# Optimization experiments

Hardware: AMD Instinct MI355X
Metric: run time of the kernel (lower is better)

The kernel has to match this reference:

```python
import jax, jax.numpy as jnp
import numpy as np

NC = 2            # num_classes
CONF_THR = 0.7
IOU_THR = 0.2

_PI, _PJ = np.triu_indices(9, k=1)   # 36 candidate edge directions for min-area rect


def _decode_level(out, stride):
    # out: [C,h,w]; scale (x,y) channels by stride and add the pixel grid, flatten to [h*w, C]
    C, h, w = out.shape
    gw = (stride * jnp.arange(w, dtype=out.dtype))[None, :]
    gh = (stride * jnp.arange(h, dtype=out.dtype))[:, None]
    out = out.at[NC + 1].set(out[NC + 1] * stride + gw)
    out = out.at[NC + 2].set(out[NC + 2] * stride + gh)
    return out.reshape(C, -1).T


def _min_area_polygons(pts18):
    # pts18: (N,18) interleaved (a,b) coordinate pairs of 9 points.
    # Min-area enclosing rectangle: optimal rect is aligned with some point-pair direction;
    # brute-force all 36 pairs (superset of hull edges) -> exact result, fully vectorized.
    P = pts18.reshape(-1, 9, 2)                       # (N,9,2)
    d = P[:, _PJ] - P[:, _PI]                         # (N,36,2)
    nrm = jnp.sqrt(jnp.sum(d * d, -1) + 1e-12)
    c, s = d[..., 0] / nrm, d[..., 1] / nrm           # (N,36)
    a, b = P[..., 0][:, None, :], P[..., 1][:, None, :]   # (N,1,9)
    u = a * c[..., None] + b * s[..., None]           # rotate by -theta
    v = -a * s[..., None] + b * c[..., None]
    umin, umax = u.min(-1), u.max(-1)
    vmin, vmax = v.min(-1), v.max(-1)
    area = (umax - umin) * (vmax - vmin)              # (N,36)
    k = jnp.argmin(area, 1)[:, None]
    tk = lambda z: jnp.take_along_axis(z, k, 1)[:, 0]
    c, s, umin, umax, vmin, vmax = map(tk, (c, s, umin, umax, vmin, vmax))
    cu = jnp.stack([umin, umax, umax, umin], -1)      # rect corners in rotated frame
    cv = jnp.stack([vmin, vmin, vmax, vmax], -1)
    ca = cu * c[:, None] - cv * s[:, None]            # rotate back
    cb = cu * s[:, None] + cv * c[:, None]
    return jnp.stack([ca, cb], -1).reshape(-1, 8)     # (N,8) interleaved corners


def _points_in_quad(pts, quad):
    # pts (M,2), quad (4,2) convex with consistent winding -> (M,) bool
    e = jnp.roll(quad, -1, 0) - quad
    r = pts[:, None, :] - quad[None]
    cr = e[None, :, 0] * r[..., 1] - e[None, :, 1] * r[..., 0]
    return (cr >= 0).all(-1) | (cr <= 0).all(-1)


def _box_decoder(rect):
    # rect (N,8) -> (N,5) [cx, cy, w, h, angle]; y_first=True convention from the source
    w = jnp.sqrt((rect[:, 0] - rect[:, 2]) ** 2 + (rect[:, 1] - rect[:, 3]) ** 2)
    h = jnp.sqrt((rect[:, 4] - rect[:, 2]) ** 2 + (rect[:, 5] - rect[:, 3]) ** 2)
    cx = rect[:, 1:8:2].sum(1) * 0.25
    cy = rect[:, 0:8:2].sum(1) * 0.25
    ang = jnp.arctan((rect[:, 0] - rect[:, 2]) / (rect[:, 1] - rect[:, 3]))
    return jnp.stack([cx, cy, w, h, ang], -1)


def _rbox_corners(b):
    cx, cy, w, h, a = b[0], b[1], b[2], b[3], b[4]
    cs, sn = jnp.cos(a), jnp.sin(a)
    lx = jnp.array([-0.5, 0.5, 0.5, -0.5]) * w
    ly = jnp.array([-0.5, -0.5, 0.5, 0.5]) * h
    return jnp.stack([cx + lx * cs - ly * sn, cy + lx * sn + ly * cs], -1)  # (4,2)


def _quad_inter_area(A, B):
    # exact intersection area of two convex quads A,B (4,2):
    # candidates = corners of each inside the other + all 16 edge-edge intersections,
    # sorted by angle around their centroid, masked shoelace.
    inA = _points_in_quad(B, A)
    inB = _points_in_quad(A, B)
    rA = jnp.roll(A, -1, 0) - A
    rB = jnp.roll(B, -1, 0) - B
    qp = B[None] - A[:, None]                                  # (4,4,2)
    den = rA[:, None, 0] * rB[None, :, 1] - rA[:, None, 1] * rB[None, :, 0]
    dsafe = jnp.where(jnp.abs(den) < 1e-9, 1e-9, den)
    t = (qp[..., 0] * rB[None, :, 1] - qp[..., 1] * rB[None, :, 0]) / dsafe
    uu = (qp[..., 0] * rA[:, None, 1] - qp[..., 1] * rA[:, None, 0]) / dsafe
    okx = (jnp.abs(den) > 1e-9) & (t >= 0) & (t <= 1) & (uu >= 0) & (uu <= 1)
    X = A[:, None] + t[..., None] * rA[:, None]
    pts = jnp.concatenate([A, B, X.reshape(16, 2)], 0)          # (24,2)
    val = jnp.concatenate([inB, inA, okx.reshape(16)], 0)
    n = val.sum()
    cen = jnp.sum(jnp.where(val[:, None], pts, 0.0), 0) / jnp.maximum(n, 1)
    rel = pts - cen
    ang = jnp.where(val, jnp.arctan2(rel[:, 1], rel[:, 0]), 1e9)
    o = jnp.argsort(ang)
    rp, vs = rel[o], val[o]
    rp = jnp.where(vs[:, None], rp, rp[0])   # invalid slots -> first valid vertex (zero-area edges)
    nx = jnp.roll(rp, -1, 0)
    area = 0.5 * jnp.abs(jnp.sum(rp[:, 0] * nx[:, 1] - rp[:, 1] * nx[:, 0]))
    return jnp.where(n >= 3, area, 0.0)


def _forward(out3, out4, out5, off1_l3, off1_l4, off1_l5, offf_l3, offf_l4, offf_l5):
    outs = jnp.concatenate([_decode_level(out3[0], 4),
                            _decode_level(out4[0], 8),
                            _decode_level(out5[0], 16)], 0)          # (N, NC+3)
    flat = lambda z: z[0].reshape(18, -1).T
    off1 = jnp.concatenate([flat(off1_l3), flat(off1_l4), flat(off1_l5)], 0)
    offf = jnp.concatenate([flat(offf_l3), flat(offf_l4), flat(offf_l5)], 0) + off1
    N = outs.shape[0]
    x, y = outs[:, NC + 1], outs[:, NC + 2]
    offf = offf + jnp.tile(jnp.stack([y, x], -1), (1, 9))            # (y,x) interleaved, 9 points
    xs, ys = offf[:, 1:18:2], offf[:, 0:18:2]
    area = (xs.max(1) - xs.min(1)) * (ys.max(1) - ys.min(1)) / 40.0
    conf = outs[:, 0]
    conf_mask = conf > CONF_THR * jax.nn.sigmoid(area)
    rect = _min_area_polygons(offf)                                  # (N,8)
    boxes5 = _box_decoder(rect)                                      # (N,5)
    corners = jax.vmap(_rbox_corners)(boxes5)                        # (N,4,2)
    areas5 = boxes5[:, 2] * boxes5[:, 3]
    position = outs[:, NC + 1:]                                      # (N,2) = (x,y)
    pts_yx = jnp.stack([position[:, 1], position[:, 0]], -1)         # (y,x), matches rect plane
    quads = rect.reshape(N, 4, 2)
    order = jnp.argsort(jnp.where(conf_mask, conf, -jnp.inf))[::-1]

    def step(carry, i):
        suppressed, keep = carry
        active = jnp.logical_not(suppressed[i])
        keep = keep.at[i].set(active)
        inside = _points_in_quad(pts_yx, quads[i])                   # points_in_polygons
        inter = jax.vmap(lambda C: _quad_inter_area(corners[i], C))(corners)
        iou = inter / (areas5[i] + areas5 - inter + 1e-9)            # box_iou_rotated
        suppressed = suppressed | (active & (inside | (iou >= IOU_THR)))
        return (suppressed, keep), None

    init = (jnp.logical_not(conf_mask), jnp.zeros(N, dtype=bool))
    (_, keep), _ = jax.lax.scan(step, init, order)

    cls = outs[:, 1:NC + 1]
    maxc = cls.max(1)
    masks = jnp.stack([keep & (cls[:, i] == maxc) for i in range(NC)], 0)  # (NC,N)
    cnt = masks.sum(1)
    result = jnp.where(masks[:, :, None], position[None], 0.0)             # (NC,N,2) padded
    rect_out = rect * keep[:, None].astype(rect.dtype)                     # (N,8) padded
    return cnt, result, rect_out


def setup_inputs() -> dict:
    key = jax.random.key(0)
    shapes = [("out3", (1, NC + 3, 32, 32)), ("out4", (1, NC + 3, 16, 16)), ("out5", (1, NC + 3, 8, 8)),
              ("off1_l3", (1, 18, 32, 32)), ("off1_l4", (1, 18, 16, 16)), ("off1_l5", (1, 18, 8, 8)),
              ("offf_l3", (1, 18, 32, 32)), ("offf_l4", (1, 18, 16, 16)), ("offf_l5", (1, 18, 8, 8))]
    ks = jax.random.split(key, len(shapes))
    return {n: jax.random.normal(k, s, dtype=jnp.float32) for (n, s), k in zip(shapes, ks)}


def reference(out3, out4, out5, off1_l3, off1_l4, off1_l5, offf_l3, offf_l4, offf_l5):
    return _forward(out3, out4, out5, off1_l3, off1_l4, off1_l5, offf_l3, offf_l4, offf_l5)
```

## Files before the change

### kernel.cpp

```cpp
#include <hip/hip_runtime.h>
#include <math.h>

#define N_DET 1344
#define NW 21
#define MW_MAX 8
#define T2S 9
#define PAIR_CAP 40000


__device__ __forceinline__ bool pt_in_quad4(const float* qx, const float* qy,
                                            float px, float py) {
    bool allp = true, alln = true;
#pragma unroll
    for (int k = 0; k < 4; k++) {
        int k1 = (k + 1) & 3;
        float ex = qx[k1] - qx[k], ey = qy[k1] - qy[k];
        float rx = px - qx[k],     ry = py - qy[k];
        float cr = ex * ry - ey * rx;
        allp = allp && (cr >= 0.f);
        alln = alln && (cr <= 0.f);
    }
    return allp || alln;
}

__device__ float quad_inter_area(const float* Ax, const float* Ay,
                                 const float* Bx, const float* By) {
    float px[24], py[24];
    unsigned vmask = 0;
    int n = 0;
#pragma unroll
    for (int k = 0; k < 4; k++) {
        px[k] = Ax[k]; py[k] = Ay[k];
        if (pt_in_quad4(Bx, By, Ax[k], Ay[k])) { vmask |= 1u << k; n++; }
    }
#pragma unroll
    for (int k = 0; k < 4; k++) {
        px[4 + k] = Bx[k]; py[4 + k] = By[k];
        if (pt_in_quad4(Ax, Ay, Bx[k], By[k])) { vmask |= 1u << (4 + k); n++; }
    }
#pragma unroll
    for (int k = 0; k < 4; k++) {
        int k1 = (k + 1) & 3;
        float rax = Ax[k1] - Ax[k], ray = Ay[k1] - Ay[k];
#pragma unroll
        for (int l = 0; l < 4; l++) {
            int l1 = (l + 1) & 3;
            float rbx = Bx[l1] - Bx[l], rby = By[l1] - By[l];
            float qpx = Bx[l] - Ax[k],  qpy = By[l] - Ay[k];
            float den = rax * rby - ray * rbx;
            float ad  = fabsf(den);
            float dsafe = (ad < 1e-9f) ? 1e-9f : den;
            float t = (qpx * rby - qpy * rbx) / dsafe;
            float u = (qpx * ray - qpy * rax) / dsafe;
            bool ok = (ad > 1e-9f) && t >= 0.f && t <= 1.f && u >= 0.f && u <= 1.f;
            int id = 8 + k * 4 + l;
            px[id] = Ax[k] + t * rax;
            py[id] = Ay[k] + t * ray;
            if (ok) { vmask |= 1u << id; n++; }
        }
    }
    float cx = 0.f, cy = 0.f;
#pragma unroll
    for (int m = 0; m < 24; m++)
        if ((vmask >> m) & 1u) { cx += px[m]; cy += py[m]; }
    int mx = (n < 1) ? 1 : n;
    cx = cx / (float)mx;
    cy = cy / (float)mx;

    unsigned long long key[32];
    float sx[32], sy[32];
#pragma unroll
    for (int m = 0; m < 24; m++) {
        float rx = px[m] - cx, ry = py[m] - cy;
        float a = ((vmask >> m) & 1u) ? atan2f(ry, rx) : 1e9f;
        unsigned u = __float_as_uint(a);
        u = (u & 0x80000000u) ? ~u : (u | 0x80000000u);
        key[m] = (((unsigned long long)u) << 6) | (unsigned)m;
        sx[m] = rx; sy[m] = ry;
    }
#pragma unroll
    for (int m = 24; m < 32; m++) { key[m] = ~0ull; sx[m] = 0.f; sy[m] = 0.f; }

#pragma unroll
    for (int k = 2; k <= 32; k <<= 1) {
#pragma unroll
        for (int j = k >> 1; j > 0; j >>= 1) {
#pragma unroll
            for (int t = 0; t < 32; t++) {
                int l = t ^ j;
                if (l > t) {
                    bool up = ((t & k) == 0);
                    bool sw = up ? (key[t] > key[l]) : (key[t] < key[l]);
                    if (sw) {
                        unsigned long long tk = key[t]; key[t] = key[l]; key[l] = tk;
                        float tx = sx[t]; sx[t] = sx[l]; sx[l] = tx;
                        float ty = sy[t]; sy[t] = sy[l]; sy[l] = ty;
                    }
                }
            }
        }
    }

    unsigned ut = __float_as_uint(1e9f) | 0x80000000u;
    unsigned long long kt = ((unsigned long long)ut) << 6;
    float fx = sx[0], fy = sy[0];
    float qx2[24], qy2[24];
#pragma unroll
    for (int m = 0; m < 24; m++) {
        bool v = key[m] < kt;
        qx2[m] = v ? sx[m] : fx;
        qy2[m] = v ? sy[m] : fy;
    }
    float ssum = 0.f;
#pragma unroll
    for (int m = 0; m < 24; m++) {
        int m1 = (m + 1) % 24;
        ssum += qx2[m] * qy2[m1] - qy2[m] * qx2[m1];
    }
    float area = 0.5f * fabsf(ssum);
    return (n >= 3) ? area : 0.f;
}

__device__ bool iou_suppress(const float* __restrict__ cor, const float* __restrict__ a5,
                             int i, int j) {
    float Axr[4], Ayr[4], Bxr[4], Byr[4];
#pragma unroll
    for (int k = 0; k < 4; k++) {
        Axr[k] = cor[i * 8 + 2 * k]; Ayr[k] = cor[i * 8 + 2 * k + 1];
        Bxr[k] = cor[j * 8 + 2 * k]; Byr[k] = cor[j * 8 + 2 * k + 1];
    }
    float inter = quad_inter_area(Axr, Ayr, Bxr, Byr);
    float iou = inter / (a5[i] + a5[j] - inter + 1e-9f);
    return iou >= 0.2f;
}

__global__ void k_decode(const float* __restrict__ out3, const float* __restrict__ out4,
                         const float* __restrict__ out5,
                         const float* __restrict__ o1l3, const float* __restrict__ o1l4,
                         const float* __restrict__ o1l5,
                         const float* __restrict__ ofl3, const float* __restrict__ ofl4,
                         const float* __restrict__ ofl5,
                         float* conf, float* cls0, float* cls1, float* xx, float* yy,
                         float* a5, float* ccx, float* ccy, float* rr,
                         float* rect, float* cor, int* mask, int* Mcnt, int* pairCnt) {
    int n = blockIdx.x * blockDim.x + threadIdx.x;
    if (n >= N_DET) return;
    if (n == 0) { *Mcnt = 0; *pairCnt = 0; }
    const float *out, *o1, *of;
    int w, idx; float stride;
    if (n < 1024)      { out = out3; o1 = o1l3; of = ofl3; w = 32; idx = n;        stride = 4.f; }
    else if (n < 1280) { out = out4; o1 = o1l4; of = ofl4; w = 16; idx = n - 1024; stride = 8.f; }
    else               { out = out5; o1 = o1l5; of = ofl5; w = 8;  idx = n - 1280; stride = 16.f; }
    int hw = w * w;
    int row = idx / w, col = idx % w;
    float cf = out[0 * hw + idx];
    float c0 = out[1 * hw + idx];
    float c1 = out[2 * hw + idx];
    float x  = out[3 * hw + idx] * stride + stride * (float)col;
    float y  = out[4 * hw + idx] * stride + stride * (float)row;

    float Pa[9], Pb[9];
    float minb = INFINITY, maxb = -INFINITY, mina = INFINITY, maxa = -INFINITY;
#pragma unroll
    for (int k = 0; k < 9; k++) {
        float a = of[(2 * k) * hw + idx]     + o1[(2 * k) * hw + idx]     + y;
        float b = of[(2 * k + 1) * hw + idx] + o1[(2 * k + 1) * hw + idx] + x;
        Pa[k] = a; Pb[k] = b;
        mina = fminf(mina, a); maxa = fmaxf(maxa, a);
        minb = fminf(minb, b); maxb = fmaxf(maxb, b);
    }
    float area = (maxb - minb) * (maxa - mina) / 40.0f;
    float sg = 1.0f / (1.0f + expf(-area));
    int m = (cf > 0.7f * sg) ? 1 : 0;

    float best = INFINITY, bc = 0.f, bs = 0.f;
    float bumin = 0.f, bumax = 0.f, bvmin = 0.f, bvmax = 0.f;
#pragma unroll
    for (int i = 0; i < 9; i++) {
#pragma unroll
        for (int j = i + 1; j < 9; j++) {
            float d0 = Pa[j] - Pa[i], d1 = Pb[j] - Pb[i];
            float nr = sqrtf(d0 * d0 + d1 * d1 + 1e-12f);
            float c = d0 / nr, s = d1 / nr;
            float umin = INFINITY, umax = -INFINITY, vmin = INFINITY, vmax = -INFINITY;
#pragma unroll
            for (int k = 0; k < 9; k++) {
                float u =  Pa[k] * c + Pb[k] * s;
                float v = -Pa[k] * s + Pb[k] * c;
                umin = fminf(umin, u); umax = fmaxf(umax, u);
                vmin = fminf(vmin, v); vmax = fmaxf(vmax, v);
            }
            float ar = (umax - umin) * (vmax - vmin);
            if (ar < best) { best = ar; bc = c; bs = s;
                             bumin = umin; bumax = umax; bvmin = vmin; bvmax = vmax; }
        }
    }
    float cu[4] = {bumin, bumax, bumax, bumin};
    float cv[4] = {bvmin, bvmin, bvmax, bvmax};
    float r8[8];
#pragma unroll
    for (int k = 0; k < 4; k++) {
        r8[2 * k]     = cu[k] * bc - cv[k] * bs;
        r8[2 * k + 1] = cu[k] * bs + cv[k] * bc;
    }
    float w5 = sqrtf((r8[0] - r8[2]) * (r8[0] - r8[2]) + (r8[1] - r8[3]) * (r8[1] - r8[3]));
    float h5 = sqrtf((r8[4] - r8[2]) * (r8[4] - r8[2]) + (r8[5] - r8[3]) * (r8[5] - r8[3]));
    float cx = (r8[1] + r8[3] + r8[5] + r8[7]) * 0.25f;
    float cy = (r8[0] + r8[2] + r8[4] + r8[6]) * 0.25f;
    float ang = atanf((r8[0] - r8[2]) / (r8[1] - r8[3]));
    float cs = cosf(ang), sn = sinf(ang);
    const float lxs[4] = {-0.5f, 0.5f, 0.5f, -0.5f};
    const float lys[4] = {-0.5f, -0.5f, 0.5f, 0.5f};
#pragma unroll
    for (int k = 0; k < 4; k++) {
        cor[n * 8 + 2 * k]     = cx + lxs[k] * w5 * cs - lys[k] * h5 * sn;
        cor[n * 8 + 2 * k + 1] = cy + lxs[k] * w5 * sn + lys[k] * h5 * cs;
    }
#pragma unroll
    for (int k = 0; k < 8; k++) rect[n * 8 + k] = r8[k];
    conf[n] = cf; cls0[n] = c0; cls1[n] = c1;
    xx[n] = x; yy[n] = y; a5[n] = w5 * h5; mask[n] = m;
    ccx[n] = cx; ccy[n] = cy;
    rr[n] = 0.5f * sqrtf(w5 * w5 + h5 * h5);
}

__global__ __launch_bounds__(64) void k_order(const float* __restrict__ conf,
                                              const int* __restrict__ mask,
                                              int* order, int* Mcnt) {
    int b = blockIdx.x;
    int lane = threadIdx.x;
    int mb = mask[b];
    float ki = mb ? conf[b] : -INFINITY;
    int rank = 0;
    for (int j = lane; j < N_DET; j += 64) {
        float kj = mask[j] ? conf[j] : -INFINITY;
        rank += ((kj > ki) || (kj == ki && j > b)) ? 1 : 0;
    }
    for (int off = 32; off; off >>= 1) rank += __shfl_down(rank, off, 64);
    if (lane == 0) {
        order[rank] = b;
        if (mb) atomicAdd(Mcnt, 1);
    }
}

__global__ __launch_bounds__(256) void k_pairs_a(
        const float* __restrict__ rect, const float* __restrict__ cor,
        const float* __restrict__ a5,
        const float* __restrict__ xx, const float* __restrict__ yy,
        const float* __restrict__ ccx, const float* __restrict__ ccy,
        const float* __restrict__ rr,
        const int* __restrict__ order, const int* __restrict__ Mcnt,
        unsigned long long* __restrict__ S2, unsigned int* __restrict__ pairs,
        int* __restrict__ pairCnt) {
    int M = *Mcnt;
    if (M <= 0) return;
    int MW = (M + 63) >> 6;
    bool use_list = (MW <= MW_MAX);
    int lane  = threadIdx.x & 63;
    int gwave = (blockIdx.x * 256 + threadIdx.x) >> 6;
    int nwave = (gridDim.x * 256) >> 6;
    int total = M * MW;
    for (int t = gwave; t < total; t += nwave) {
        int p = t / MW;
        int w = t - p * MW;
        int i = order[p];
        int q = w * 64 + lane;
        bool valid = q < M;
        int j = valid ? order[q] : i;

        float cbi = ccx[i], cai = ccy[i], ri = rr[i];
        float da = yy[j] - cai, db = xx[j] - cbi;
        float rin = ri + 0.1f;
        bool inside = false;
        if (da * da + db * db <= rin * rin) {
            float qxr[4], qyr[4];
#pragma unroll
            for (int k = 0; k < 4; k++) { qxr[k] = rect[i * 8 + 2 * k]; qyr[k] = rect[i * 8 + 2 * k + 1]; }
            inside = pt_in_quad4(qxr, qyr, yy[j], xx[j]);
        }
        bool bit = valid && inside;
        unsigned long long bb = __ballot(bit);
        if (lane == 0) S2[p * MW + w] = bb;

        float ex = cbi - ccx[j], ey = cai - ccy[j];
        float rs = ri + rr[j] + 0.1f;
        bool iou_pos = valid && (q != p) && !bit && (ex * ex + ey * ey <= rs * rs);
        if (use_list) {
            unsigned long long pm = __ballot(iou_pos);
            if (pm) {
                int cw = __popcll(pm);
                int base = 0;
                if (lane == 0) base = atomicAdd(pairCnt, cw);
                base = __shfl(base, 0, 64);
                if (iou_pos) {
                    int pos = base + __popcll(pm & ((1ull << lane) - 1ull));
                    if (pos < PAIR_CAP) {
                        pairs[pos] = ((unsigned)p << 11) | (unsigned)q;
                    } else if (iou_suppress(cor, a5, i, j)) {
                        atomicOr(&S2[p * MW + w], 1ull << (q & 63));
                    }
                }
            }
        } else if (iou_pos) {
            if (iou_suppress(cor, a5, i, j))
                atomicOr(&S2[p * MW + w], 1ull << (q & 63));
        }
    }
}

__global__ __launch_bounds__(256) void k_pairs_b(
        const float* __restrict__ cor, const float* __restrict__ a5,
        const int* __restrict__ order, const int* __restrict__ Mcnt,
        const int* __restrict__ pairCnt, const unsigned int* __restrict__ pairs,
        unsigned long long* __restrict__ S2) {
    int M = *Mcnt;
    int MW = (M + 63) >> 6;
    if (MW > MW_MAX) return;
    int cnt = *pairCnt; if (cnt > PAIR_CAP) cnt = PAIR_CAP;
    int stride = gridDim.x * 256;
    for (int t = blockIdx.x * 256 + threadIdx.x; t < cnt; t += stride) {
        unsigned v = pairs[t];
        int p = (int)(v >> 11), q = (int)(v & 2047u);
        int i = order[p], j = order[q];
        if (iou_suppress(cor, a5, i, j))
            atomicOr(&S2[p * MW + (q >> 6)], 1ull << (q & 63));
    }
}

__global__ __launch_bounds__(512) void k_scan_out(
    const float* __restrict__ cls0, const float* __restrict__ cls1,
    const float* __restrict__ xx, const float* __restrict__ yy,
    const float* __restrict__ rect,
    const int* __restrict__ order, const int* __restrict__ Mcnt,
    const unsigned long long* __restrict__ S2, float* __restrict__ out) {
    __shared__ int order_s[N_DET];
    __shared__ unsigned long long T2[512 * T2S];
    __shared__ unsigned long long Kfin[MW_MAX];
    __shared__ unsigned int keep32[(N_DET + 31) / 32];
    __shared__ int cnt_s[2];
    int tid = threadIdx.x;
    int lane = tid & 63, wid = tid >> 6;
    int M = *Mcnt;
    int MW = (M + 63) >> 6;
    for (int t = tid; t < N_DET; t += 512) order_s[t] = order[t];
    for (int t = tid; t < (N_DET + 31) / 32; t += 512) keep32[t] = 0u;
    if (tid < 2) cnt_s[tid] = 0;
    if (tid < MW_MAX) Kfin[tid] = 0ull;
    __syncthreads();

    if (M > 0 && MW <= MW_MAX) {
        for (int blk = wid; blk < MW * MW; blk += 8) {
            int wp = blk / MW, wq = blk - wp * MW;
            int pp = wp * 64 + lane;
            unsigned long long x = (pp < M) ? S2[pp * MW + wq] : 0ull;
#pragma unroll
            for (int b = 0; b < 64; b++) {
                unsigned long long bb = __ballot((x >> b) & 1ull);
                if (lane == b) T2[(wq * 64 + b) * T2S + wp] = bb;
            }
        }
        __syncthreads();

        if (wid == 0) {
            unsigned long long kw[MW_MAX];
#pragma unroll
            for (int w = 0; w < MW_MAX; w++) {
                int lo = w * 64;
                kw[w] = (M > lo) ? ((M - lo >= 64) ? ~0ull : ((1ull << (M - lo)) - 1ull)) : 0ull;
            }
            unsigned long long pmask = lane ? ((1ull << lane) - 1ull) : 0ull;
            for (int it = 0; it <= M; ++it) {
                bool changed = false;
#pragma unroll
                for (int k = 0; k < MW_MAX; k++) {
                    if (k < MW) {
                        int q = k * 64 + lane;
                        const unsigned long long* row = &T2[q * T2S];
                        unsigned long long sup = 0ull;
#pragma unroll
                        for (int w = 0; w < MW_MAX; w++) {
                            if (w < k)       sup |= row[w] & kw[w];
                            else if (w == k) sup |= row[w] & kw[w] & pmask;
                        }
                        bool nb = (q < M) && (sup == 0ull);
                        unsigned long long nw = __ballot(nb);
                        changed |= (nw != kw[k]);
                        kw[k] = nw;
                    }
                }
                if (!changed) break;
            }
            if (lane == 0) {
#pragma unroll
                for (int w = 0; w < MW_MAX; w++) Kfin[w] = kw[w];
            }
        }
        __syncthreads();
        for (int t = tid; t < M; t += 512) {
            if ((Kfin[t >> 6] >> (t & 63)) & 1ull) {
                int i = order_s[t];
                atomicOr(&keep32[i >> 5], 1u << (i & 31));
            }
        }
    } else if (M > 0) {
        if (wid == 0) {
            unsigned long long rem = 0ull;
            int lo = lane * 64;
            if (M > lo) rem = (M - lo >= 64) ? ~0ull : ((1ull << (M - lo)) - 1ull);
            for (int guard = 0; guard < N_DET; guard++) {
                unsigned long long vote = __ballot(rem != 0ull);
                if (!vote) break;
                int w = __builtin_ctzll(vote);
                unsigned long long wd = __shfl(rem, w, 64);
                int b = __builtin_ctzll(wd);
                int p = w * 64 + b;
                int i = order_s[p];
                if (lane == 0) atomicOr(&keep32[i >> 5], 1u << (i & 31));
                unsigned long long rowv = (lane < MW) ? S2[p * MW + lane] : 0ull;
                rem &= ~rowv;
                if (lane == w) rem &= ~(1ull << b);
            }
        }
    }
    __syncthreads();

    int c0 = 0, c1 = 0;
    for (int n = tid; n < N_DET; n += 512) {
        bool kp = (keep32[n >> 5] >> (n & 31)) & 1u;
        float a = cls0[n], b = cls1[n];
        float mxc = fmaxf(a, b);
        bool m0 = kp && (a == mxc);
        bool m1 = kp && (b == mxc);
        float x = xx[n], y = yy[n];
        out[2 + 0 * N_DET * 2 + n * 2 + 0] = m0 ? x : 0.f;
        out[2 + 0 * N_DET * 2 + n * 2 + 1] = m0 ? y : 0.f;
        out[2 + 1 * N_DET * 2 + n * 2 + 0] = m1 ? x : 0.f;
        out[2 + 1 * N_DET * 2 + n * 2 + 1] = m1 ? y : 0.f;
        float kf = kp ? 1.f : 0.f;
#pragma unroll
        for (int k = 0; k < 8; k++)
            out[2 + 2 * N_DET * 2 + n * 8 + k] = rect[n * 8 + k] * kf;
        c0 += m0 ? 1 : 0;
        c1 += m1 ? 1 : 0;
    }
    if (c0) atomicAdd(&cnt_s[0], c0);
    if (c1) atomicAdd(&cnt_s[1], c1);
    __syncthreads();
    if (tid == 0) { out[0] = (float)cnt_s[0]; out[1] = (float)cnt_s[1]; }
}

extern "C" void kernel_launch(void* const* d_in, const int* in_sizes, int n_in,
                              void* d_out, int out_size, void* d_ws, size_t ws_size,
                              hipStream_t stream) {
    const float* out3 = (const float*)d_in[0];
    const float* out4 = (const float*)d_in[1];
    const float* out5 = (const float*)d_in[2];
    const float* o1l3 = (const float*)d_in[3];
    const float* o1l4 = (const float*)d_in[4];
    const float* o1l5 = (const float*)d_in[5];
    const float* ofl3 = (const float*)d_in[6];
    const float* ofl4 = (const float*)d_in[7];
    const float* ofl5 = (const float*)d_in[8];
    float* out = (float*)d_out;

    const int N = N_DET;
    float* wsf  = (float*)d_ws;
    float* conf = wsf + 0 * N;
    float* cls0 = wsf + 1 * N;
    float* cls1 = wsf + 2 * N;
    float* xx   = wsf + 3 * N;
    float* yy   = wsf + 4 * N;
    float* a5   = wsf + 5 * N;
    float* ccx  = wsf + 6 * N;
    float* ccy  = wsf + 7 * N;
    float* rr   = wsf + 8 * N;
    float* rect = wsf + 9 * N;
    float* cor  = wsf + 17 * N;
    int* mask   = (int*)(wsf + 25 * N);
    int* order  = mask + N;
    int* Mcnt   = order + N;
    int* pairCnt = Mcnt + 1;
    unsigned long long* S2 = (unsigned long long*)(wsf + 27 * N + 4);
    unsigned int* pairs = (unsigned int*)((char*)S2 + 32768);

    k_decode<<<(N + 255) / 256, 256, 0, stream>>>(out3, out4, out5, o1l3, o1l4, o1l5,
                                                  ofl3, ofl4, ofl5,
                                                  conf, cls0, cls1, xx, yy, a5,
                                                  ccx, ccy, rr, rect, cor, mask, Mcnt, pairCnt);
    k_order<<<N, 64, 0, stream>>>(conf, mask, order, Mcnt);
    k_pairs_a<<<1024, 256, 0, stream>>>(rect, cor, a5, xx, yy, ccx, ccy, rr,
                                        order, Mcnt, S2, pairs, pairCnt);
    k_pairs_b<<<64, 256, 0, stream>>>(cor, a5, order, Mcnt, pairCnt, pairs, S2);
    k_scan_out<<<1, 512, 0, stream>>>(cls0, cls1, xx, yy, rect, order, Mcnt, S2, out);
}
```

Before: 142.9 us.

## Scatter per-box data into sorted order and fuse pair kernels via shared-memory queue

The sort kernel now also scatters box attributes (centers, radii, areas, rects, corners) into rank-ordered compacted arrays, so the pair kernel indexes them directly instead of going through order[] indirection. The two pair kernels are merged into one: candidate IoU pairs are queued in a per-block shared-memory queue and evaluated after a block barrier rather than through a global list processed by a second launch. The grid drops from 1024 to 256 blocks, and the mask is folded into a single key array. This removes one launch, the global pair buffer and its atomic counter, at the cost of extra scatter writes in the sort kernel and the risk that a block's queue overflows into inline evaluation.

```diff
diff --git a/kernel.cpp b/kernel.cpp
--- a/kernel.cpp
+++ b/kernel.cpp
@@ -2,10 +2,9 @@
 #include <math.h>
 
 #define N_DET 1344
-#define NW 21
 #define MW_MAX 8
 #define T2S 9
-#define PAIR_CAP 40000
+#define QCAP 2048
 
 
 __device__ __forceinline__ bool pt_in_quad4(const float* qx, const float* qy,
@@ -121,16 +120,16 @@
     return (n >= 3) ? area : 0.f;
 }
 
-__device__ bool iou_suppress(const float* __restrict__ cor, const float* __restrict__ a5,
-                             int i, int j) {
+__device__ bool iou_suppress_c(const float* __restrict__ co_cor,
+                               const float* __restrict__ co_a5, int p, int q) {
     float Axr[4], Ayr[4], Bxr[4], Byr[4];
 #pragma unroll
     for (int k = 0; k < 4; k++) {
-        Axr[k] = cor[i * 8 + 2 * k]; Ayr[k] = cor[i * 8 + 2 * k + 1];
-        Bxr[k] = cor[j * 8 + 2 * k]; Byr[k] = cor[j * 8 + 2 * k + 1];
+        Axr[k] = co_cor[p * 8 + 2 * k]; Ayr[k] = co_cor[p * 8 + 2 * k + 1];
+        Bxr[k] = co_cor[q * 8 + 2 * k]; Byr[k] = co_cor[q * 8 + 2 * k + 1];
     }
     float inter = quad_inter_area(Axr, Ayr, Bxr, Byr);
-    float iou = inter / (a5[i] + a5[j] - inter + 1e-9f);
+    float iou = inter / (co_a5[p] + co_a5[q] - inter + 1e-9f);
     return iou >= 0.2f;
 }
 
@@ -140,12 +139,12 @@
                          const float* __restrict__ o1l5,
                          const float* __restrict__ ofl3, const float* __restrict__ ofl4,
                          const float* __restrict__ ofl5,
-                         float* conf, float* cls0, float* cls1, float* xx, float* yy,
+                         float* keyArr, float* cls0, float* cls1, float* xx, float* yy,
                          float* a5, float* ccx, float* ccy, float* rr,
-                         float* rect, float* cor, int* mask, int* Mcnt, int* pairCnt) {
+                         float* rect, float* cor, int* Mcnt) {
     int n = blockIdx.x * blockDim.x + threadIdx.x;
     if (n >= N_DET) return;
-    if (n == 0) { *Mcnt = 0; *pairCnt = 0; }
+    if (n == 0) *Mcnt = 0;
     const float *out, *o1, *of;
     int w, idx; float stride;
     if (n < 1024)      { out = out3; o1 = o1l3; of = ofl3; w = 32; idx = n;        stride = 4.f; }
@@ -218,112 +217,128 @@
     }
 #pragma unroll
     for (int k = 0; k < 8; k++) rect[n * 8 + k] = r8[k];
-    conf[n] = cf; cls0[n] = c0; cls1[n] = c1;
-    xx[n] = x; yy[n] = y; a5[n] = w5 * h5; mask[n] = m;
+    keyArr[n] = m ? cf : -INFINITY;
+    cls0[n] = c0; cls1[n] = c1;
+    xx[n] = x; yy[n] = y; a5[n] = w5 * h5;
     ccx[n] = cx; ccy[n] = cy;
     rr[n] = 0.5f * sqrtf(w5 * w5 + h5 * h5);
 }
 
-__global__ __launch_bounds__(64) void k_order(const float* __restrict__ conf,
-                                              const int* __restrict__ mask,
-                                              int* order, int* Mcnt) {
+__global__ __launch_bounds__(64) void k_order(
+        const float* __restrict__ keyArr,
+        const float* __restrict__ xx, const float* __restrict__ yy,
+        const float* __restrict__ a5, const float* __restrict__ ccx,
+        const float* __restrict__ ccy, const float* __restrict__ rr,
+        const float* __restrict__ rect, const float* __restrict__ cor,
+        int* order, int* Mcnt,
+        float* co_ccx, float* co_ccy, float* co_rr, float* co_a5,
+        float* co_xx, float* co_yy, float* co_rect, float* co_cor) {
     int b = blockIdx.x;
     int lane = threadIdx.x;
-    int mb = mask[b];
-    float ki = mb ? conf[b] : -INFINITY;
+    float ki = keyArr[b];
     int rank = 0;
     for (int j = lane; j < N_DET; j += 64) {
-        float kj = mask[j] ? conf[j] : -INFINITY;
+        float kj = keyArr[j];
         rank += ((kj > ki) || (kj == ki && j > b)) ? 1 : 0;
     }
     for (int off = 32; off; off >>= 1) rank += __shfl_down(rank, off, 64);
+    rank = __shfl(rank, 0, 64);
     if (lane == 0) {
         order[rank] = b;
-        if (mb) atomicAdd(Mcnt, 1);
-    }
-}
-
-__global__ __launch_bounds__(256) void k_pairs_a(
-        const float* __restrict__ rect, const float* __restrict__ cor,
-        const float* __restrict__ a5,
-        const float* __restrict__ xx, const float* __restrict__ yy,
-        const float* __restrict__ ccx, const float* __restrict__ ccy,
-        const float* __restrict__ rr,
-        const int* __restrict__ order, const int* __restrict__ Mcnt,
-        unsigned long long* __restrict__ S2, unsigned int* __restrict__ pairs,
-        int* __restrict__ pairCnt) {
+        if (ki != -INFINITY) atomicAdd(Mcnt, 1);
+    }
+    if (lane < 8)            co_cor[rank * 8 + lane]        = cor[b * 8 + lane];
+    else if (lane < 16)      co_rect[rank * 8 + (lane - 8)] = rect[b * 8 + (lane - 8)];
+    else if (lane == 16)     co_ccx[rank] = ccx[b];
+    else if (lane == 17)     co_ccy[rank] = ccy[b];
+    else if (lane == 18)     co_rr[rank]  = rr[b];
+    else if (lane == 19)     co_a5[rank]  = a5[b];
+    else if (lane == 20)     co_xx[rank]  = xx[b];
+    else if (lane == 21)     co_yy[rank]  = yy[b];
+}
+
+__global__ __launch_bounds__(256) void k_pairs(
+        const float* __restrict__ co_rect, const float* __restrict__ co_cor,
+        const float* __restrict__ co_a5,
+        const float* __restrict__ co_xx, const float* __restrict__ co_yy,
+        const float* __restrict__ co_ccx, const float* __restrict__ co_ccy,
+        const float* __restrict__ co_rr,
+        const int* __restrict__ Mcnt, unsigned long long* __restrict__ S2) {
+    __shared__ unsigned int queue[QCAP];
+    __shared__ int qn;
     int M = *Mcnt;
-    if (M <= 0) return;
     int MW = (M + 63) >> 6;
-    bool use_list = (MW <= MW_MAX);
-    int lane  = threadIdx.x & 63;
-    int gwave = (blockIdx.x * 256 + threadIdx.x) >> 6;
-    int nwave = (gridDim.x * 256) >> 6;
-    int total = M * MW;
-    for (int t = gwave; t < total; t += nwave) {
-        int p = t / MW;
-        int w = t - p * MW;
-        int i = order[p];
-        int q = w * 64 + lane;
-        bool valid = q < M;
-        int j = valid ? order[q] : i;
-
-        float cbi = ccx[i], cai = ccy[i], ri = rr[i];
-        float da = yy[j] - cai, db = xx[j] - cbi;
-        float rin = ri + 0.1f;
-        bool inside = false;
-        if (da * da + db * db <= rin * rin) {
-            float qxr[4], qyr[4];
-#pragma unroll
-            for (int k = 0; k < 4; k++) { qxr[k] = rect[i * 8 + 2 * k]; qyr[k] = rect[i * 8 + 2 * k + 1]; }
-            inside = pt_in_quad4(qxr, qyr, yy[j], xx[j]);
-        }
-        bool bit = valid && inside;
-        unsigned long long bb = __ballot(bit);
-        if (lane == 0) S2[p * MW + w] = bb;
-
-        float ex = cbi - ccx[j], ey = cai - ccy[j];
-        float rs = ri + rr[j] + 0.1f;
-        bool iou_pos = valid && (q != p) && !bit && (ex * ex + ey * ey <= rs * rs);
-        if (use_list) {
-            unsigned long long pm = __ballot(iou_pos);
-            if (pm) {
-                int cw = __popcll(pm);
-                int base = 0;
-                if (lane == 0) base = atomicAdd(pairCnt, cw);
-                base = __shfl(base, 0, 64);
-                if (iou_pos) {
-                    int pos = base + __popcll(pm & ((1ull << lane) - 1ull));
-                    if (pos < PAIR_CAP) {
-                        pairs[pos] = ((unsigned)p << 11) | (unsigned)q;
-                    } else if (iou_suppress(cor, a5, i, j)) {
-                        atomicOr(&S2[p * MW + w], 1ull << (q & 63));
+    bool fast = (MW <= MW_MAX);
+    int tid = threadIdx.x;
+    int lane = tid & 63;
+    if (tid == 0) qn = 0;
+    __syncthreads();
+
+    if (M > 0) {
+        int gwave = (blockIdx.x * 256 + tid) >> 6;
+        int nwave = (gridDim.x * 256) >> 6;
+        int total = M * MW;
+        for (int t = gwave; t < total; t += nwave) {
+            int p = t / MW;
+            int w = t - p * MW;
+            int q = w * 64 + lane;
+            bool valid = q < M;
+            int qc = valid ? q : 0;
+
+            float cbi = co_ccx[p], cai = co_ccy[p], ri = co_rr[p];
+            float pjy = co_yy[qc], pjx = co_xx[qc];
+            float da = pjy - cai, db = pjx - cbi;
+            float rin = ri + 0.1f;
+            bool inside = false;
+            if (da * da + db * db <= rin * rin) {
+                float qxr[4], qyr[4];
+#pragma unroll
+                for (int k = 0; k < 4; k++) { qxr[k] = co_rect[p * 8 + 2 * k]; qyr[k] = co_rect[p * 8 + 2 * k + 1]; }
+                inside = pt_in_quad4(qxr, qyr, pjy, pjx);
+            }
+            bool bit = valid && inside;
+            unsigned long long bb = __ballot(bit);
+
+            float ex = cbi - co_ccx[qc], ey = cai - co_ccy[qc];
+            float rs = ri + co_rr[qc] + 0.1f;
+            bool needy = valid && (q != p) && !bit && (ex * ex + ey * ey <= rs * rs);
+
+            if (fast) {
+                if (lane == 0) S2[p * MW + w] = bb;
+                unsigned long long pm = __ballot(needy);
+                if (pm) {
+                    int cw = __popcll(pm);
+                    int base = 0;
+                    if (lane == 0) base = atomicAdd(&qn, cw);
+                    base = __shfl(base, 0, 64);
+                    if (needy) {
+                        int pos = base + __popcll(pm & ((1ull << lane) - 1ull));
+                        if (pos < QCAP) {
+                            queue[pos] = ((unsigned)p << 11) | (unsigned)q;
+                        } else {
+                            __threadfence();
+                            if (iou_suppress_c(co_cor, co_a5, p, q))
+                                atomicOr(&S2[p * MW + w], 1ull << (q & 63));
+                        }
                     }
                 }
-            }
-        } else if (iou_pos) {
-            if (iou_suppress(cor, a5, i, j))
-                atomicOr(&S2[p * MW + w], 1ull << (q & 63));
-        }
-    }
-}
-
-__global__ __launch_bounds__(256) void k_pairs_b(
-        const float* __restrict__ cor, const float* __restrict__ a5,
-        const int* __restrict__ order, const int* __restrict__ Mcnt,
-        const int* __restrict__ pairCnt, const unsigned int* __restrict__ pairs,
-        unsigned long long* __restrict__ S2) {
-    int M = *Mcnt;
-    int MW = (M + 63) >> 6;
-    if (MW > MW_MAX) return;
-    int cnt = *pairCnt; if (cnt > PAIR_CAP) cnt = PAIR_CAP;
-    int stride = gridDim.x * 256;
-    for (int t = blockIdx.x * 256 + threadIdx.x; t < cnt; t += stride) {
-        unsigned v = pairs[t];
-        int p = (int)(v >> 11), q = (int)(v & 2047u);
-        int i = order[p], j = order[q];
-        if (iou_suppress(cor, a5, i, j))
-            atomicOr(&S2[p * MW + (q >> 6)], 1ull << (q & 63));
+            } else {
+                bool supp = needy && iou_suppress_c(co_cor, co_a5, p, q);
+                unsigned long long sb = __ballot(supp);
+                if (lane == 0) S2[p * MW + w] = bb | sb;
+            }
+        }
+    }
+    __syncthreads();
+
+    if (M > 0 && fast) {
+        int cnt = qn; if (cnt > QCAP) cnt = QCAP;
+        for (int t = tid; t < cnt; t += 256) {
+            unsigned v = queue[t];
+            int p = (int)(v >> 11), q = (int)(v & 2047u);
+            if (iou_suppress_c(co_cor, co_a5, p, q))
+                atomicOr(&S2[p * MW + (q >> 6)], 1ull << (q & 63));
+        }
     }
 }
 
@@ -333,7 +348,6 @@
     const float* __restrict__ rect,
     const int* __restrict__ order, const int* __restrict__ Mcnt,
     const unsigned long long* __restrict__ S2, float* __restrict__ out) {
-    __shared__ int order_s[N_DET];
     __shared__ unsigned long long T2[512 * T2S];
     __shared__ unsigned long long Kfin[MW_MAX];
     __shared__ unsigned int keep32[(N_DET + 31) / 32];
@@ -342,7 +356,6 @@
     int lane = tid & 63, wid = tid >> 6;
     int M = *Mcnt;
     int MW = (M + 63) >> 6;
-    for (int t = tid; t < N_DET; t += 512) order_s[t] = order[t];
     for (int t = tid; t < (N_DET + 31) / 32; t += 512) keep32[t] = 0u;
     if (tid < 2) cnt_s[tid] = 0;
     if (tid < MW_MAX) Kfin[tid] = 0ull;
@@ -398,7 +411,7 @@
         __syncthreads();
         for (int t = tid; t < M; t += 512) {
             if ((Kfin[t >> 6] >> (t & 63)) & 1ull) {
-                int i = order_s[t];
+                int i = order[t];
                 atomicOr(&keep32[i >> 5], 1u << (i & 31));
             }
         }
@@ -414,7 +427,7 @@
                 unsigned long long wd = __shfl(rem, w, 64);
                 int b = __builtin_ctzll(wd);
                 int p = w * 64 + b;
-                int i = order_s[p];
+                int i = order[p];
                 if (lane == 0) atomicOr(&keep32[i >> 5], 1u << (i & 31));
                 unsigned long long rowv = (lane < MW) ? S2[p * MW + lane] : 0ull;
                 rem &= ~rowv;
@@ -452,6 +465,9 @@
 extern "C" void kernel_launch(void* const* d_in, const int* in_sizes, int n_in,
                               void* d_out, int out_size, void* d_ws, size_t ws_size,
                               hipStream_t stream) {
+    const int N = N_DET;
+    float* wsf = (float*)d_ws;
+
     const float* out3 = (const float*)d_in[0];
     const float* out4 = (const float*)d_in[1];
     const float* out5 = (const float*)d_in[2];
@@ -463,33 +479,38 @@
     const float* ofl5 = (const float*)d_in[8];
     float* out = (float*)d_out;
 
-    const int N = N_DET;
-    float* wsf  = (float*)d_ws;
-    float* conf = wsf + 0 * N;
-    float* cls0 = wsf + 1 * N;
-    float* cls1 = wsf + 2 * N;
-    float* xx   = wsf + 3 * N;
-    float* yy   = wsf + 4 * N;
-    float* a5   = wsf + 5 * N;
-    float* ccx  = wsf + 6 * N;
-    float* ccy  = wsf + 7 * N;
-    float* rr   = wsf + 8 * N;
-    float* rect = wsf + 9 * N;
-    float* cor  = wsf + 17 * N;
-    int* mask   = (int*)(wsf + 25 * N);
-    int* order  = mask + N;
-    int* Mcnt   = order + N;
-    int* pairCnt = Mcnt + 1;
-    unsigned long long* S2 = (unsigned long long*)(wsf + 27 * N + 4);
-    unsigned int* pairs = (unsigned int*)((char*)S2 + 32768);
+    float* keyArr = wsf + 0 * N;
+    float* cls0   = wsf + 1 * N;
+    float* cls1   = wsf + 2 * N;
+    float* xx     = wsf + 3 * N;
+    float* yy     = wsf + 4 * N;
+    float* a5     = wsf + 5 * N;
+    float* ccx    = wsf + 6 * N;
+    float* ccy    = wsf + 7 * N;
+    float* rr     = wsf + 8 * N;
+    float* rect   = wsf + 9 * N;
+    float* cor    = wsf + 17 * N;
+    float* co_ccx = wsf + 25 * N;
+    float* co_ccy = wsf + 26 * N;
+    float* co_rr  = wsf + 27 * N;
+    float* co_a5  = wsf + 28 * N;
+    float* co_xx  = wsf + 29 * N;
+    float* co_yy  = wsf + 30 * N;
+    float* co_rect= wsf + 31 * N;
+    float* co_cor = wsf + 39 * N;
+    int* order    = (int*)(wsf + 47 * N);
+    int* Mcnt     = order + N;
+    unsigned long long* S2 = (unsigned long long*)(wsf + 48 * N + 8);
 
     k_decode<<<(N + 255) / 256, 256, 0, stream>>>(out3, out4, out5, o1l3, o1l4, o1l5,
                                                   ofl3, ofl4, ofl5,
-                                                  conf, cls0, cls1, xx, yy, a5,
-                                                  ccx, ccy, rr, rect, cor, mask, Mcnt, pairCnt);
-    k_order<<<N, 64, 0, stream>>>(conf, mask, order, Mcnt);
-    k_pairs_a<<<1024, 256, 0, stream>>>(rect, cor, a5, xx, yy, ccx, ccy, rr,
-                                        order, Mcnt, S2, pairs, pairCnt);
-    k_pairs_b<<<64, 256, 0, stream>>>(cor, a5, order, Mcnt, pairCnt, pairs, S2);
+                                                  keyArr, cls0, cls1, xx, yy, a5,
+                                                  ccx, ccy, rr, rect, cor, Mcnt);
+    k_order<<<N, 64, 0, stream>>>(keyArr, xx, yy, a5, ccx, ccy, rr, rect, cor,
+                                  order, Mcnt,
+                                  co_ccx, co_ccy, co_rr, co_a5, co_xx, co_yy,
+                                  co_rect, co_cor);
+    k_pairs<<<256, 256, 0, stream>>>(co_rect, co_cor, co_a5, co_xx, co_yy,
+                                     co_ccx, co_ccy, co_rr, Mcnt, S2);
     k_scan_out<<<1, 512, 0, stream>>>(cls0, cls1, xx, yy, rect, order, Mcnt, S2, out);
 }
```

Measured after the change: 127.8 us. 1.12x faster.
